# Kernel optimization log

Hardware: AMD Instinct MI355X
Metric: run time of the kernel (lower is better)

The kernel has to match this reference:

```python
import jax, jax.numpy as jnp
import numpy as np

EPS = 1e-7  # eps used inside bbox_iou
LAMBDA_BBOX = 1.0
LAMBDA_CLS = 1.0


def _coords(b):
    x, y, w, h = b[..., 0], b[..., 1], b[..., 2], b[..., 3]
    return x - w / 2, y - h / 2, x + w / 2, y + h / 2


def _pairwise_giou_loss(pred, target):
    # pred [B,T,4] -> [B,T,1,4]; target [B,O,4] -> [B,1,O,4]; broadcast to [B,T,O]
    b1x1, b1y1, b1x2, b1y2 = _coords(pred[:, :, None, :])
    b2x1, b2y1, b2x2, b2y2 = _coords(target[:, None, :, :])
    w1, h1 = b1x2 - b1x1, b1y2 - b1y1 + EPS
    w2, h2 = b2x2 - b2x1, b2y2 - b2y1 + EPS
    inter = jnp.clip(jnp.minimum(b1x2, b2x2) - jnp.maximum(b1x1, b2x1), 0) * \
            jnp.clip(jnp.minimum(b1y2, b2y2) - jnp.maximum(b1y1, b2y1), 0)
    union = w1 * h1 + w2 * h2 - inter + EPS
    iou = inter / union
    cw = jnp.maximum(b1x2, b2x2) - jnp.minimum(b1x1, b2x1)
    ch = jnp.maximum(b1y2, b2y2) - jnp.minimum(b1y1, b2y1)
    c_area = cw * ch + EPS
    giou = iou - (c_area - union) / c_area
    return 1.0 - giou  # [B,T,O]


def _lsa_rows(c):
    # Jonker-Volgenant shortest augmenting path (same algorithm as scipy's
    # linear_sum_assignment). c is [n, m] with n <= m; returns col4row [n].
    n, m = c.shape
    u = np.zeros(n)
    v = np.zeros(m)
    col4row = np.full(n, -1, np.int64)
    row4col = np.full(m, -1, np.int64)
    for cur in range(n):
        shortest = np.full(m, np.inf)
        path = np.full(m, -1, np.int64)
        SR = np.zeros(n, bool)
        SC = np.zeros(m, bool)
        min_val = 0.0
        i = cur
        sink = -1
        while sink == -1:
            SR[i] = True
            r = min_val + c[i] - u[i] - v
            upd = (~SC) & (r < shortest)
            shortest[upd] = r[upd]
            path[upd] = i
            masked = np.where(SC, np.inf, shortest)
            j = int(np.argmin(masked))
            min_val = masked[j]
            SC[j] = True
            if row4col[j] == -1:
                sink = j
            else:
                i = row4col[j]
        u[cur] += min_val
        sr = SR.copy(); sr[cur] = False
        u[sr] += min_val - shortest[col4row[sr]]
        v[SC] -= min_val - shortest[SC]
        j = sink
        while True:
            i = path[j]
            row4col[j] = i
            col4row[i], j = j, col4row[i]
            if i == cur:
                break
    return col4row


def _hungarian_np(cost):
    # Host callback; sequential per-batch like the original scipy loop.
    cost = np.asarray(cost, np.float64)
    B, T, O = cost.shape
    pred_idx = np.zeros((B, O), np.int32)
    tgt_idx = np.zeros((B, O), np.int32)
    for b in range(B):
        col4row = _lsa_rows(cost[b].T)  # assign each target (O rows) a token
        order = np.argsort(col4row)      # sort by pred index like scipy output
        pred_idx[b] = col4row[order].astype(np.int32)
        tgt_idx[b] = order.astype(np.int32)
    return pred_idx, tgt_idx


def _cost_matrix(pred_bboxes, target_bboxes, pred_classes, target_classes):
    B, T, C = pred_classes.shape
    O = target_classes.shape[1]
    log_probs = jax.nn.log_softmax(pred_classes, axis=-1)              # [B,T,C]
    idx = jnp.broadcast_to(target_classes[:, None, :], (B, T, O))      # [B,T,O]
    cls_neg_log = -jnp.take_along_axis(log_probs, idx, axis=-1)        # [B,T,O]
    ciou_loss = _pairwise_giou_loss(pred_bboxes, target_bboxes)        # [B,T,O]
    return LAMBDA_BBOX * ciou_loss + LAMBDA_CLS * cls_neg_log


def setup_inputs() -> dict:
    key = jax.random.key(0)
    k1, k2, k3, k4 = jax.random.split(key, 4)
    B, T, O, C = 32, 2048, 128, 80
    return {
        "pred_bboxes": jax.random.uniform(k1, (B, T, 4), dtype=jnp.float32),
        "target_bboxes": jax.random.uniform(k2, (B, O, 4), dtype=jnp.float32),
        "pred_classes": jax.random.normal(k3, (B, T, C), dtype=jnp.float32),
        "target_classes": jax.random.randint(k4, (B, O), 0, C, dtype=jnp.int32),
    }


def reference(pred_bboxes, target_bboxes, pred_classes, target_classes):
    cost = _cost_matrix(pred_bboxes, target_bboxes, pred_classes, target_classes)
    B, _, O = cost.shape
    out_spec = (jax.ShapeDtypeStruct((B, O), jnp.int32),
                jax.ShapeDtypeStruct((B, O), jnp.int32))
    pred_idx, tgt_idx = jax.pure_callback(_hungarian_np, out_spec, cost)
    return pred_idx, tgt_idx
```

## Files before the change

### kernel.cpp

```cpp
#include <hip/hip_runtime.h>
#include <math.h>
#include <float.h>

#define BB 32
#define TT 2048
#define OO 128
#define CC 80
#define EPSF 1e-7f
#define NT 256
#define SLOTS 8
#define CPAD 81
#define TPT 128
#define NTILE 16

typedef float vf4 __attribute__((ext_vector_type(4)));

struct alignas(16) URow { double u; int row; int pad; };
struct alignas(8)  P2   { int i; int j; };
struct alignas(16) Cand { double v; double u; int j; int row; };

template<int CTRL>
__device__ __forceinline__ void dpp_lexmin(double& bv, int& bj) {
    int lo = __double2loint(bv), hi = __double2hiint(bv);
    int tlo = __builtin_amdgcn_update_dpp(0, lo, CTRL, 0xF, 0xF, false);
    int thi = __builtin_amdgcn_update_dpp(0x7FF00000, hi, CTRL, 0xF, 0xF, false);
    int tj  = __builtin_amdgcn_update_dpp(0x7FFFFFFF, bj, CTRL, 0xF, 0xF, false);
    double tv = __hiloint2double(thi, tlo);
    if (tv <= bv) { bv = tv; bj = tj; }
}

template<int CTRL>
__device__ __forceinline__ void dpp_lexmin_f32(float& bv, int& bj) {
    int tlo = __builtin_amdgcn_update_dpp(0x7F800000, __float_as_int(bv), CTRL, 0xF, 0xF, false);
    int tj  = __builtin_amdgcn_update_dpp(0x7FFFFFFF, bj, CTRL, 0xF, 0xF, false);
    float tv = __int_as_float(tlo);
    if (tv < bv || (tv == bv && tj < bj)) { bv = tv; bj = tj; }
}

union SM {
    struct {
        float  xv[TPT * CPAD];
        float4 box[OO];
        float2 wt[OO];
        unsigned long long rmin[OO * 2];
    } c;
    struct {
        URow   urow[TT];
        P2     path2[TT];
        int    row4col[TT];
        int    claim[TT];
        int    col4row[OO];
        double u[OO];
        int    amin[OO];
        int    flag[OO];
        int    freelist[OO];
        int    selj[OO + 8];
        double selm[OO + 8];
        int    selrow[OO + 8];
        Cand   cand[2][4];
        int    nfree;
    } l;
};

__global__ __launch_bounds__(NT) void hung_fused_kernel(
    const float* __restrict__ pb, const float* __restrict__ tb,
    const float* __restrict__ cls, const int* __restrict__ tcls,
    float* __restrict__ cost, unsigned long long* __restrict__ rowmins,
    int* __restrict__ cnt, int* __restrict__ out) {
#pragma clang fp contract(off)
    __shared__ SM sm;

    int bx = blockIdx.x;
    int b = bx & 31;
    int tile = bx >> 5;
    int t0 = tile * TPT;
    int tid = threadIdx.x;
    int lane = tid & 63;
    int wave = tid >> 6;
    int tok = tid & (TPT - 1);
    int oh = tid >> 7;

    {
        const float* cbase = cls + ((size_t)b * TT + t0) * CC;
        #pragma unroll
        for (int k = 0; k < (TPT * CC) / (NT * 4); ++k) {
            int idx4 = (k * NT + tid) * 4;
            vf4 vv = __builtin_nontemporal_load((const vf4*)(cbase + idx4));
            int r = idx4 / CC;
            int c = idx4 - r * CC;
            float* dst = &sm.c.xv[r * CPAD + c];
            dst[0] = vv.x; dst[1] = vv.y; dst[2] = vv.z; dst[3] = vv.w;
        }
        if (tid < OO) {
            float4 tbox = ((const float4*)tb)[b * OO + tid];
            float x1 = tbox.x - tbox.z / 2.f;
            float y1 = tbox.y - tbox.w / 2.f;
            float x2 = tbox.x + tbox.z / 2.f;
            float y2 = tbox.y + tbox.w / 2.f;
            float4 bb; bb.x = x1; bb.y = y1; bb.z = x2; bb.w = y2;
            sm.c.box[tid] = bb;
            float w2 = x2 - x1;
            float h2 = (y2 - y1) + EPSF;
            float2 wt; wt.x = w2 * h2;
            wt.y = __int_as_float(tcls[b * OO + tid]);
            sm.c.wt[tid] = wt;
        }
        __syncthreads();

        size_t bt = (size_t)b * TT + t0 + tok;
        float4 pbox = ((const float4*)pb)[bt];
        float b1x1 = pbox.x - pbox.z / 2.f;
        float b1y1 = pbox.y - pbox.w / 2.f;
        float b1x2 = pbox.x + pbox.z / 2.f;
        float b1y2 = pbox.y + pbox.w / 2.f;
        float w1 = b1x2 - b1x1;
        float h1 = (b1y2 - b1y1) + EPSF;
        float w1h1 = w1 * h1;

        const float* xr = &sm.c.xv[tok * CPAD];
        float m = xr[0];
        #pragma unroll
        for (int c = 1; c < CC; ++c) m = fmaxf(m, xr[c]);
        float ssum = 0.f;
        #pragma unroll
        for (int c = 0; c < CC; ++c) ssum += expf(xr[c] - m);
        float ls = logf(ssum);

        float* cbt = cost + (size_t)b * OO * TT + t0;
        for (int k = 0; k < OO / 2; ++k) {
            int o = oh * (OO / 2) + k;
            float4 bb = sm.c.box[o];
            float2 wt = sm.c.wt[o];
            float b2x1 = bb.x, b2y1 = bb.y, b2x2 = bb.z, b2y2 = bb.w;
            float iw = fminf(b1x2, b2x2) - fmaxf(b1x1, b2x1);
            float ih = fminf(b1y2, b2y2) - fmaxf(b1y1, b2y1);
            iw = fmaxf(iw, 0.f);
            ih = fmaxf(ih, 0.f);
            float inter = iw * ih;
            float uni = ((w1h1 + wt.x) - inter) + EPSF;
            float iou = inter / uni;
            float cw = fmaxf(b1x2, b2x2) - fminf(b1x1, b2x1);
            float ch = fmaxf(b1y2, b2y2) - fminf(b1y1, b2y1);
            float c_area = (cw * ch) + EPSF;
            float giou = iou - (c_area - uni) / c_area;
            float bbox_loss = 1.0f - giou;

            float xc = xr[__float_as_int(wt.y)];
            float shifted = xc - m;
            float cls_neg = -(shifted - ls);

            float cval = bbox_loss + cls_neg;
            cbt[(size_t)o * TT + tok] = cval;

            float bvv = cval;
            int bjj = t0 + tok;
            dpp_lexmin_f32<0x111>(bvv, bjj);
            dpp_lexmin_f32<0x112>(bvv, bjj);
            dpp_lexmin_f32<0x114>(bvv, bjj);
            dpp_lexmin_f32<0x118>(bvv, bjj);
            dpp_lexmin_f32<0x142>(bvv, bjj);
            dpp_lexmin_f32<0x143>(bvv, bjj);
            if (lane == 63)
                sm.c.rmin[o * 2 + (wave & 1)] =
                    ((unsigned long long)__float_as_uint(bvv) << 32) | (unsigned)bjj;
        }
        __syncthreads();
        if (tid < OO) {
            unsigned long long r0 = sm.c.rmin[tid * 2 + 0];
            unsigned long long r1 = sm.c.rmin[tid * 2 + 1];
            rowmins[((size_t)b * NTILE + tile) * OO + tid] = r0 < r1 ? r0 : r1;
        }
        __syncthreads();
        if (tid == 0)
            __hip_atomic_fetch_add(&cnt[b], 1, __ATOMIC_RELEASE,
                                   __HIP_MEMORY_SCOPE_AGENT);
    }

    if (tile != 0) return;

    if (tid == 0) {
        while (__hip_atomic_load(&cnt[b], __ATOMIC_ACQUIRE,
                                 __HIP_MEMORY_SCOPE_AGENT) < NTILE)
            __builtin_amdgcn_s_sleep(2);
    }
    __syncthreads();

    const float* cb = cost + (size_t)b * OO * TT;
    const int jbase = tid * SLOTS;

    double v_[SLOTS];
    double key[SLOTS];
    #pragma unroll
    for (int s = 0; s < SLOTS; ++s) v_[s] = 0.0;

    if (tid < OO) {
        const unsigned long long* p = rowmins + (size_t)b * NTILE * OO + tid;
        unsigned long long best = p[0];
        #pragma unroll
        for (int t = 1; t < NTILE; ++t) {
            unsigned long long x = p[t * OO];
            if (x < best) best = x;
        }
        sm.l.u[tid] = (double)__uint_as_float((unsigned)(best >> 32));
        sm.l.amin[tid] = (int)(best & 0xFFFFFFFFull);
        sm.l.col4row[tid] = -1;
    }
    for (int j = tid; j < TT; j += NT) { sm.l.row4col[j] = -1; sm.l.claim[j] = 0x7FFFFFFF; }
    __syncthreads();

    if (tid < OO) atomicMin(&sm.l.claim[sm.l.amin[tid]], tid);
    __syncthreads();
    if (tid < OO) {
        int j = sm.l.amin[tid];
        if (sm.l.claim[j] == tid) { sm.l.col4row[tid] = j; sm.l.row4col[j] = tid; }
    }
    __syncthreads();

    for (int j = tid; j < TT; j += NT) {
        int r = sm.l.row4col[j];
        URow t; t.row = r; t.u = (r >= 0) ? sm.l.u[r] : 0.0; t.pad = 0;
        sm.l.urow[j] = t;
    }
    if (tid < OO) sm.l.flag[tid] = (sm.l.col4row[tid] < 0) ? 1 : 0;
    __syncthreads();
    if (tid < OO && sm.l.flag[tid]) {
        int rank = 0;
        for (int o = 0; o < tid; ++o) rank += sm.l.flag[o];
        sm.l.freelist[rank] = tid;
    }
    if (tid == 0) {
        int nf = 0;
        for (int o = 0; o < OO; ++o) nf += sm.l.flag[o];
        sm.l.nfree = nf;
    }
    __syncthreads();
    int nfree = sm.l.nfree;

    float4 pf0, pf1;
    if (nfree > 0) {
        const float* rr = cb + (size_t)sm.l.freelist[0] * TT + jbase;
        pf0 = *(const float4*)rr;
        pf1 = *(const float4*)(rr + 4);
    }

    int par = 0;
    for (int fi = 0; fi < nfree; ++fi) {
        int cur = sm.l.freelist[fi];

        #pragma unroll
        for (int s = 0; s < SLOTS; ++s) key[s] = INFINITY;
        int selbits = 0;
        double mv = 0.0;
        int i = cur, jc = -1;
        double ui = sm.l.u[cur];
        float4 c0 = pf0, c1 = pf1;
        int L = 0, sink;

        while (true) {
            float cv[SLOTS] = {c0.x, c0.y, c0.z, c0.w, c1.x, c1.y, c1.z, c1.w};
            double D = ui - mv;

            double bv = INFINITY;
            int bj = TT;
            #pragma unroll
            for (int s = 0; s < SLOTS; ++s) {
                if (!((selbits >> s) & 1)) {
                    double r = ((double)cv[s] - D) - v_[s];
                    if (r < key[s]) {
                        key[s] = r;
                        P2 p; p.i = i; p.j = jc;
                        sm.l.path2[s * NT + tid] = p;
                    }
                    double kk = key[s];
                    if (kk < bv) { bv = kk; bj = jbase + s; }
                }
            }
            dpp_lexmin<0x111>(bv, bj);
            dpp_lexmin<0x112>(bv, bj);
            dpp_lexmin<0x114>(bv, bj);
            dpp_lexmin<0x118>(bv, bj);
            dpp_lexmin<0x142>(bv, bj);
            dpp_lexmin<0x143>(bv, bj);
            int rlo = __builtin_amdgcn_readlane(__double2loint(bv), 63);
            int rhi = __builtin_amdgcn_readlane(__double2hiint(bv), 63);
            double wv = __hiloint2double(rhi, rlo);
            int wj = __builtin_amdgcn_readlane(bj, 63);

            URow uwv = sm.l.urow[wj];

            par ^= 1;
            if (lane == 0) {
                Cand c; c.v = wv; c.u = uwv.u; c.j = wj; c.row = uwv.row;
                sm.l.cand[par][wave] = c;
            }
            __syncthreads();

            Cand cc0 = sm.l.cand[par][0];
            Cand cc1 = sm.l.cand[par][1];
            Cand cc2 = sm.l.cand[par][2];
            Cand cc3 = sm.l.cand[par][3];
            double MV = cc0.v; int BJ = cc0.j; int WR = cc0.row; double WU = cc0.u;
            if (cc1.v < MV || (cc1.v == MV && cc1.j < BJ)) { MV = cc1.v; BJ = cc1.j; WR = cc1.row; WU = cc1.u; }
            if (cc2.v < MV || (cc2.v == MV && cc2.j < BJ)) { MV = cc2.v; BJ = cc2.j; WR = cc2.row; WU = cc2.u; }
            if (cc3.v < MV || (cc3.v == MV && cc3.j < BJ)) { MV = cc3.v; BJ = cc3.j; WR = cc3.row; WU = cc3.u; }
            mv = MV;
            if ((BJ >> 3) == tid) selbits |= 1 << (BJ & 7);
            if (tid == 0) sm.l.selj[L] = BJ;

            if (WR < 0) { sink = BJ; break; }
            if (tid == 0) { sm.l.selm[L] = MV; sm.l.selrow[L] = WR; }
            i = WR; ui = WU; jc = BJ;
            L++;
            const float* crow = cb + (size_t)i * TT + jbase;
            c0 = *(const float4*)crow;
            c1 = *(const float4*)(crow + 4);
        }

        if (fi + 1 < nfree) {
            const float* rr = cb + (size_t)sm.l.freelist[fi + 1] * TT + jbase;
            pf0 = *(const float4*)rr;
            pf1 = *(const float4*)(rr + 4);
        }

        double M = mv;
        #pragma unroll
        for (int s = 0; s < SLOTS; ++s)
            if ((selbits >> s) & 1) v_[s] = v_[s] - (M - key[s]);
        for (int k = tid; k < L; k += NT)
            sm.l.u[sm.l.selrow[k]] = sm.l.u[sm.l.selrow[k]] + (M - sm.l.selm[k]);
        if (tid == 0) {
            sm.l.u[cur] = sm.l.u[cur] + M;
            int j = sink;
            while (true) {
                P2 p = sm.l.path2[(j & 7) * NT + (j >> 3)];
                int ii = p.i;
                sm.l.row4col[j] = ii;
                sm.l.col4row[ii] = j;
                if (ii == cur) break;
                j = p.j;
            }
        }
        __syncthreads();
        if (tid <= L) {
            int j = sm.l.selj[tid];
            int r = sm.l.row4col[j];
            URow t; t.u = sm.l.u[r]; t.row = r; t.pad = 0;
            sm.l.urow[j] = t;
        }
        __syncthreads();
    }

    if (tid < OO) {
        int my = sm.l.col4row[tid];
        int rank = 0;
        for (int o = 0; o < OO; ++o) rank += (sm.l.col4row[o] < my) ? 1 : 0;
        out[(size_t)b * OO + rank] = my;
        out[(size_t)(BB + b) * OO + rank] = tid;
    }
}

extern "C" void kernel_launch(void* const* d_in, const int* in_sizes, int n_in,
                              void* d_out, int out_size, void* d_ws, size_t ws_size,
                              hipStream_t stream) {
    const float* pred_bboxes = (const float*)d_in[0];
    const float* target_bboxes = (const float*)d_in[1];
    const float* pred_classes = (const float*)d_in[2];
    const int* target_classes = (const int*)d_in[3];
    int* out = (int*)d_out;

    float* cost = (float*)d_ws;
    unsigned long long* rowmins =
        (unsigned long long*)(cost + (size_t)BB * OO * TT);
    int* cnt = (int*)(rowmins + (size_t)BB * NTILE * OO);

    (void)hipMemsetAsync(cnt, 0, BB * sizeof(int), stream);

    hung_fused_kernel<<<BB * NTILE, NT, 0, stream>>>(
        pred_bboxes, target_bboxes, pred_classes, target_classes,
        cost, rowmins, cnt, out);
}
```

Measured before the change: 260.0 us.

## Seed Hungarian init with second-min gaps and dual price adjustments

Each cost row now carries its second-smallest value alongside its minimum through the DPP reductions and the per-tile merge. When several rows share the same argmin column, the row with the largest gap to its second minimum takes that column. The winner's u and the column's v are adjusted by the largest competing gap, so the initial duals stay feasible. The aim is to start with more rows already assigned and tighter duals, which shortens the serial augmenting-path phase. In exchange the reductions do extra shuffle work and the claim step is an O(O^2) scan.

```diff
diff --git a/kernel.cpp b/kernel.cpp
--- a/kernel.cpp
+++ b/kernel.cpp
@@ -30,11 +30,14 @@
 }
 
 template<int CTRL>
-__device__ __forceinline__ void dpp_lexmin_f32(float& bv, int& bj) {
+__device__ __forceinline__ void dpp_top2_f32(float& bv, int& bj, float& sv) {
     int tlo = __builtin_amdgcn_update_dpp(0x7F800000, __float_as_int(bv), CTRL, 0xF, 0xF, false);
     int tj  = __builtin_amdgcn_update_dpp(0x7FFFFFFF, bj, CTRL, 0xF, 0xF, false);
+    int tso = __builtin_amdgcn_update_dpp(0x7F800000, __float_as_int(sv), CTRL, 0xF, 0xF, false);
     float tv = __int_as_float(tlo);
-    if (tv < bv || (tv == bv && tj < bj)) { bv = tv; bj = tj; }
+    float ts = __int_as_float(tso);
+    if (tv < bv || (tv == bv && tj < bj)) { sv = fminf(bv, ts); bv = tv; bj = tj; }
+    else sv = fminf(sv, tv);
 }
 
 union SM {
@@ -43,15 +46,18 @@
         float4 box[OO];
         float2 wt[OO];
         unsigned long long rmin[OO * 2];
+        float  rsec[OO * 2];
     } c;
     struct {
         URow   urow[TT];
         P2     path2[TT];
         int    row4col[TT];
-        int    claim[TT];
         int    col4row[OO];
         double u[OO];
+        double gapd[OO];
+        double pvv[OO];
         int    amin[OO];
+        int    pj[OO];
         int    flag[OO];
         int    freelist[OO];
         int    selj[OO + 8];
@@ -66,7 +72,7 @@
     const float* __restrict__ pb, const float* __restrict__ tb,
     const float* __restrict__ cls, const int* __restrict__ tcls,
     float* __restrict__ cost, unsigned long long* __restrict__ rowmins,
-    int* __restrict__ cnt, int* __restrict__ out) {
+    float* __restrict__ rowsec, int* __restrict__ cnt, int* __restrict__ out) {
 #pragma clang fp contract(off)
     __shared__ SM sm;
 
@@ -154,21 +160,31 @@
 
             float bvv = cval;
             int bjj = t0 + tok;
-            dpp_lexmin_f32<0x111>(bvv, bjj);
-            dpp_lexmin_f32<0x112>(bvv, bjj);
-            dpp_lexmin_f32<0x114>(bvv, bjj);
-            dpp_lexmin_f32<0x118>(bvv, bjj);
-            dpp_lexmin_f32<0x142>(bvv, bjj);
-            dpp_lexmin_f32<0x143>(bvv, bjj);
-            if (lane == 63)
+            float svv = INFINITY;
+            dpp_top2_f32<0x111>(bvv, bjj, svv);
+            dpp_top2_f32<0x112>(bvv, bjj, svv);
+            dpp_top2_f32<0x114>(bvv, bjj, svv);
+            dpp_top2_f32<0x118>(bvv, bjj, svv);
+            dpp_top2_f32<0x142>(bvv, bjj, svv);
+            dpp_top2_f32<0x143>(bvv, bjj, svv);
+            if (lane == 63) {
                 sm.c.rmin[o * 2 + (wave & 1)] =
                     ((unsigned long long)__float_as_uint(bvv) << 32) | (unsigned)bjj;
+                sm.c.rsec[o * 2 + (wave & 1)] = svv;
+            }
         }
         __syncthreads();
         if (tid < OO) {
             unsigned long long r0 = sm.c.rmin[tid * 2 + 0];
             unsigned long long r1 = sm.c.rmin[tid * 2 + 1];
-            rowmins[((size_t)b * NTILE + tile) * OO + tid] = r0 < r1 ? r0 : r1;
+            float s0 = sm.c.rsec[tid * 2 + 0];
+            float s1 = sm.c.rsec[tid * 2 + 1];
+            unsigned long long best; float sec;
+            if (r1 < r0) { best = r1; sec = fminf(s1, __uint_as_float((unsigned)(r0 >> 32))); }
+            else         { best = r0; sec = fminf(s0, __uint_as_float((unsigned)(r1 >> 32))); }
+            size_t off = ((size_t)b * NTILE + tile) * OO + tid;
+            rowmins[off] = best;
+            rowsec[off] = sec;
         }
         __syncthreads();
         if (tid == 0)
@@ -195,26 +211,58 @@
 
     if (tid < OO) {
         const unsigned long long* p = rowmins + (size_t)b * NTILE * OO + tid;
+        const float* ps = rowsec + (size_t)b * NTILE * OO + tid;
         unsigned long long best = p[0];
+        float sec = ps[0];
         #pragma unroll
         for (int t = 1; t < NTILE; ++t) {
-            unsigned long long x = p[t * OO];
-            if (x < best) best = x;
-        }
-        sm.l.u[tid] = (double)__uint_as_float((unsigned)(best >> 32));
+            unsigned long long x = p[(size_t)t * OO];
+            float xs = ps[(size_t)t * OO];
+            if (x < best) { sec = fminf(__uint_as_float((unsigned)(best >> 32)), xs); best = x; }
+            else          { sec = fminf(sec, __uint_as_float((unsigned)(x >> 32))); }
+        }
+        float m1 = __uint_as_float((unsigned)(best >> 32));
+        sm.l.u[tid] = (double)m1;
         sm.l.amin[tid] = (int)(best & 0xFFFFFFFFull);
+        sm.l.gapd[tid] = (double)sec - (double)m1;
         sm.l.col4row[tid] = -1;
     }
-    for (int j = tid; j < TT; j += NT) { sm.l.row4col[j] = -1; sm.l.claim[j] = 0x7FFFFFFF; }
+    for (int j = tid; j < TT; j += NT) sm.l.row4col[j] = -1;
     __syncthreads();
 
-    if (tid < OO) atomicMin(&sm.l.claim[sm.l.amin[tid]], tid);
+    if (tid < OO) {
+        int j1 = sm.l.amin[tid];
+        double g = sm.l.gapd[tid];
+        bool win = true;
+        double p = 0.0;
+        for (int o = 0; o < OO; ++o) {
+            if (o == tid) continue;
+            if (sm.l.amin[o] != j1) continue;
+            double go = sm.l.gapd[o];
+            if (go > g || (go == g && o < tid)) win = false;
+            else p = fmax(p, go);
+        }
+        if (win) {
+            sm.l.col4row[tid] = j1;
+            sm.l.row4col[j1] = tid;
+            sm.l.u[tid] = sm.l.u[tid] + p;
+            sm.l.pj[tid] = j1;
+            sm.l.pvv[tid] = p;
+        } else {
+            sm.l.pj[tid] = -1;
+        }
+    }
     __syncthreads();
-    if (tid < OO) {
-        int j = sm.l.amin[tid];
-        if (sm.l.claim[j] == tid) { sm.l.col4row[tid] = j; sm.l.row4col[j] = tid; }
-    }
-    __syncthreads();
+
+    for (int o = 0; o < OO; ++o) {
+        int pjo = sm.l.pj[o];
+        if ((pjo >> 3) == tid) {
+            double pv = -sm.l.pvv[o];
+            int s = pjo & 7;
+            #pragma unroll
+            for (int ss = 0; ss < SLOTS; ++ss) if (s == ss) v_[ss] = pv;
+        }
+    }
 
     for (int j = tid; j < TT; j += NT) {
         int r = sm.l.row4col[j];
@@ -371,11 +419,12 @@
     float* cost = (float*)d_ws;
     unsigned long long* rowmins =
         (unsigned long long*)(cost + (size_t)BB * OO * TT);
-    int* cnt = (int*)(rowmins + (size_t)BB * NTILE * OO);
+    float* rowsec = (float*)(rowmins + (size_t)BB * NTILE * OO);
+    int* cnt = (int*)(rowsec + (size_t)BB * NTILE * OO);
 
     (void)hipMemsetAsync(cnt, 0, BB * sizeof(int), stream);
 
     hung_fused_kernel<<<BB * NTILE, NT, 0, stream>>>(
         pred_bboxes, target_bboxes, pred_classes, target_classes,
-        cost, rowmins, cnt, out);
+        cost, rowmins, rowsec, cnt, out);
 }
```

After: 283.7 us. 9.1% more time.

## Split fused cost+assignment kernel into two launches, dropping spin-wait counters

Applied to the files above, without the earlier changes.

Splits the single fused kernel, in which tile-0 blocks spin on an atomic counter until all cost tiles finish, into a cost kernel and a separate 32-block assignment kernel launched after it. This removes the memset, the atomics and the spin-wait, and lets each kernel size its shared memory separately. Separate LDS may improve occupancy of the cost phase, since its smaller struct no longer has to match the larger union. The cost is an extra kernel launch and losing the overlap where early-finishing batches could begin assignment before other batches' cost tiles completed.

```diff
diff --git a/kernel.cpp b/kernel.cpp
--- a/kernel.cpp
+++ b/kernel.cpp
@@ -37,38 +37,19 @@
     if (tv < bv || (tv == bv && tj < bj)) { bv = tv; bj = tj; }
 }
 
-union SM {
-    struct {
-        float  xv[TPT * CPAD];
-        float4 box[OO];
-        float2 wt[OO];
-        unsigned long long rmin[OO * 2];
-    } c;
-    struct {
-        URow   urow[TT];
-        P2     path2[TT];
-        int    row4col[TT];
-        int    claim[TT];
-        int    col4row[OO];
-        double u[OO];
-        int    amin[OO];
-        int    flag[OO];
-        int    freelist[OO];
-        int    selj[OO + 8];
-        double selm[OO + 8];
-        int    selrow[OO + 8];
-        Cand   cand[2][4];
-        int    nfree;
-    } l;
+struct SMC {
+    float  xv[TPT * CPAD];
+    float4 box[OO];
+    float2 wt[OO];
+    unsigned long long rmin[OO * 2];
 };
 
-__global__ __launch_bounds__(NT) void hung_fused_kernel(
+__global__ __launch_bounds__(NT) void hung_cost_kernel(
     const float* __restrict__ pb, const float* __restrict__ tb,
     const float* __restrict__ cls, const int* __restrict__ tcls,
-    float* __restrict__ cost, unsigned long long* __restrict__ rowmins,
-    int* __restrict__ cnt, int* __restrict__ out) {
+    float* __restrict__ cost, unsigned long long* __restrict__ rowmins) {
 #pragma clang fp contract(off)
-    __shared__ SM sm;
+    __shared__ SMC sm;
 
     int bx = blockIdx.x;
     int b = bx & 31;
@@ -80,110 +61,125 @@
     int tok = tid & (TPT - 1);
     int oh = tid >> 7;
 
-    {
-        const float* cbase = cls + ((size_t)b * TT + t0) * CC;
-        #pragma unroll
-        for (int k = 0; k < (TPT * CC) / (NT * 4); ++k) {
-            int idx4 = (k * NT + tid) * 4;
-            vf4 vv = __builtin_nontemporal_load((const vf4*)(cbase + idx4));
-            int r = idx4 / CC;
-            int c = idx4 - r * CC;
-            float* dst = &sm.c.xv[r * CPAD + c];
-            dst[0] = vv.x; dst[1] = vv.y; dst[2] = vv.z; dst[3] = vv.w;
-        }
-        if (tid < OO) {
-            float4 tbox = ((const float4*)tb)[b * OO + tid];
-            float x1 = tbox.x - tbox.z / 2.f;
-            float y1 = tbox.y - tbox.w / 2.f;
-            float x2 = tbox.x + tbox.z / 2.f;
-            float y2 = tbox.y + tbox.w / 2.f;
-            float4 bb; bb.x = x1; bb.y = y1; bb.z = x2; bb.w = y2;
-            sm.c.box[tid] = bb;
-            float w2 = x2 - x1;
-            float h2 = (y2 - y1) + EPSF;
-            float2 wt; wt.x = w2 * h2;
-            wt.y = __int_as_float(tcls[b * OO + tid]);
-            sm.c.wt[tid] = wt;
-        }
-        __syncthreads();
-
-        size_t bt = (size_t)b * TT + t0 + tok;
-        float4 pbox = ((const float4*)pb)[bt];
-        float b1x1 = pbox.x - pbox.z / 2.f;
-        float b1y1 = pbox.y - pbox.w / 2.f;
-        float b1x2 = pbox.x + pbox.z / 2.f;
-        float b1y2 = pbox.y + pbox.w / 2.f;
-        float w1 = b1x2 - b1x1;
-        float h1 = (b1y2 - b1y1) + EPSF;
-        float w1h1 = w1 * h1;
-
-        const float* xr = &sm.c.xv[tok * CPAD];
-        float m = xr[0];
-        #pragma unroll
-        for (int c = 1; c < CC; ++c) m = fmaxf(m, xr[c]);
-        float ssum = 0.f;
-        #pragma unroll
-        for (int c = 0; c < CC; ++c) ssum += expf(xr[c] - m);
-        float ls = logf(ssum);
-
-        float* cbt = cost + (size_t)b * OO * TT + t0;
-        for (int k = 0; k < OO / 2; ++k) {
-            int o = oh * (OO / 2) + k;
-            float4 bb = sm.c.box[o];
-            float2 wt = sm.c.wt[o];
-            float b2x1 = bb.x, b2y1 = bb.y, b2x2 = bb.z, b2y2 = bb.w;
-            float iw = fminf(b1x2, b2x2) - fmaxf(b1x1, b2x1);
-            float ih = fminf(b1y2, b2y2) - fmaxf(b1y1, b2y1);
-            iw = fmaxf(iw, 0.f);
-            ih = fmaxf(ih, 0.f);
-            float inter = iw * ih;
-            float uni = ((w1h1 + wt.x) - inter) + EPSF;
-            float iou = inter / uni;
-            float cw = fmaxf(b1x2, b2x2) - fminf(b1x1, b2x1);
-            float ch = fmaxf(b1y2, b2y2) - fminf(b1y1, b2y1);
-            float c_area = (cw * ch) + EPSF;
-            float giou = iou - (c_area - uni) / c_area;
-            float bbox_loss = 1.0f - giou;
-
-            float xc = xr[__float_as_int(wt.y)];
-            float shifted = xc - m;
-            float cls_neg = -(shifted - ls);
-
-            float cval = bbox_loss + cls_neg;
-            cbt[(size_t)o * TT + tok] = cval;
-
-            float bvv = cval;
-            int bjj = t0 + tok;
-            dpp_lexmin_f32<0x111>(bvv, bjj);
-            dpp_lexmin_f32<0x112>(bvv, bjj);
-            dpp_lexmin_f32<0x114>(bvv, bjj);
-            dpp_lexmin_f32<0x118>(bvv, bjj);
-            dpp_lexmin_f32<0x142>(bvv, bjj);
-            dpp_lexmin_f32<0x143>(bvv, bjj);
-            if (lane == 63)
-                sm.c.rmin[o * 2 + (wave & 1)] =
-                    ((unsigned long long)__float_as_uint(bvv) << 32) | (unsigned)bjj;
-        }
-        __syncthreads();
-        if (tid < OO) {
-            unsigned long long r0 = sm.c.rmin[tid * 2 + 0];
-            unsigned long long r1 = sm.c.rmin[tid * 2 + 1];
-            rowmins[((size_t)b * NTILE + tile) * OO + tid] = r0 < r1 ? r0 : r1;
-        }
-        __syncthreads();
-        if (tid == 0)
-            __hip_atomic_fetch_add(&cnt[b], 1, __ATOMIC_RELEASE,
-                                   __HIP_MEMORY_SCOPE_AGENT);
-    }
-
-    if (tile != 0) return;
-
-    if (tid == 0) {
-        while (__hip_atomic_load(&cnt[b], __ATOMIC_ACQUIRE,
-                                 __HIP_MEMORY_SCOPE_AGENT) < NTILE)
-            __builtin_amdgcn_s_sleep(2);
-    }
-    __syncthreads();
+    const float* cbase = cls + ((size_t)b * TT + t0) * CC;
+    #pragma unroll
+    for (int k = 0; k < (TPT * CC) / (NT * 4); ++k) {
+        int idx4 = (k * NT + tid) * 4;
+        vf4 vv = __builtin_nontemporal_load((const vf4*)(cbase + idx4));
+        int r = idx4 / CC;
+        int c = idx4 - r * CC;
+        float* dst = &sm.xv[r * CPAD + c];
+        dst[0] = vv.x; dst[1] = vv.y; dst[2] = vv.z; dst[3] = vv.w;
+    }
+    if (tid < OO) {
+        float4 tbox = ((const float4*)tb)[b * OO + tid];
+        float x1 = tbox.x - tbox.z / 2.f;
+        float y1 = tbox.y - tbox.w / 2.f;
+        float x2 = tbox.x + tbox.z / 2.f;
+        float y2 = tbox.y + tbox.w / 2.f;
+        float4 bb; bb.x = x1; bb.y = y1; bb.z = x2; bb.w = y2;
+        sm.box[tid] = bb;
+        float w2 = x2 - x1;
+        float h2 = (y2 - y1) + EPSF;
+        float2 wt; wt.x = w2 * h2;
+        wt.y = __int_as_float(tcls[b * OO + tid]);
+        sm.wt[tid] = wt;
+    }
+    __syncthreads();
+
+    size_t bt = (size_t)b * TT + t0 + tok;
+    float4 pbox = ((const float4*)pb)[bt];
+    float b1x1 = pbox.x - pbox.z / 2.f;
+    float b1y1 = pbox.y - pbox.w / 2.f;
+    float b1x2 = pbox.x + pbox.z / 2.f;
+    float b1y2 = pbox.y + pbox.w / 2.f;
+    float w1 = b1x2 - b1x1;
+    float h1 = (b1y2 - b1y1) + EPSF;
+    float w1h1 = w1 * h1;
+
+    const float* xr = &sm.xv[tok * CPAD];
+    float m = xr[0];
+    #pragma unroll
+    for (int c = 1; c < CC; ++c) m = fmaxf(m, xr[c]);
+    float ssum = 0.f;
+    #pragma unroll
+    for (int c = 0; c < CC; ++c) ssum += expf(xr[c] - m);
+    float ls = logf(ssum);
+
+    float* cbt = cost + (size_t)b * OO * TT + t0;
+    for (int k = 0; k < OO / 2; ++k) {
+        int o = oh * (OO / 2) + k;
+        float4 bb = sm.box[o];
+        float2 wt = sm.wt[o];
+        float b2x1 = bb.x, b2y1 = bb.y, b2x2 = bb.z, b2y2 = bb.w;
+        float iw = fminf(b1x2, b2x2) - fmaxf(b1x1, b2x1);
+        float ih = fminf(b1y2, b2y2) - fmaxf(b1y1, b2y1);
+        iw = fmaxf(iw, 0.f);
+        ih = fmaxf(ih, 0.f);
+        float inter = iw * ih;
+        float uni = ((w1h1 + wt.x) - inter) + EPSF;
+        float iou = inter / uni;
+        float cw = fmaxf(b1x2, b2x2) - fminf(b1x1, b2x1);
+        float ch = fmaxf(b1y2, b2y2) - fminf(b1y1, b2y1);
+        float c_area = (cw * ch) + EPSF;
+        float giou = iou - (c_area - uni) / c_area;
+        float bbox_loss = 1.0f - giou;
+
+        float xc = xr[__float_as_int(wt.y)];
+        float shifted = xc - m;
+        float cls_neg = -(shifted - ls);
+
+        float cval = bbox_loss + cls_neg;
+        cbt[(size_t)o * TT + tok] = cval;
+
+        float bvv = cval;
+        int bjj = t0 + tok;
+        dpp_lexmin_f32<0x111>(bvv, bjj);
+        dpp_lexmin_f32<0x112>(bvv, bjj);
+        dpp_lexmin_f32<0x114>(bvv, bjj);
+        dpp_lexmin_f32<0x118>(bvv, bjj);
+        dpp_lexmin_f32<0x142>(bvv, bjj);
+        dpp_lexmin_f32<0x143>(bvv, bjj);
+        if (lane == 63)
+            sm.rmin[o * 2 + (wave & 1)] =
+                ((unsigned long long)__float_as_uint(bvv) << 32) | (unsigned)bjj;
+    }
+    __syncthreads();
+    if (tid < OO) {
+        unsigned long long r0 = sm.rmin[tid * 2 + 0];
+        unsigned long long r1 = sm.rmin[tid * 2 + 1];
+        rowmins[((size_t)b * NTILE + tile) * OO + tid] = r0 < r1 ? r0 : r1;
+    }
+}
+
+struct SML {
+    URow   urow[TT];
+    P2     path2[TT];
+    int    row4col[TT];
+    int    claim[TT];
+    int    col4row[OO];
+    double u[OO];
+    int    amin[OO];
+    int    flag[OO];
+    int    freelist[OO];
+    int    selj[OO + 8];
+    double selm[OO + 8];
+    int    selrow[OO + 8];
+    Cand   cand[2][4];
+    int    nfree;
+};
+
+__global__ __launch_bounds__(NT) void hung_lsa_kernel(
+    const float* __restrict__ cost,
+    const unsigned long long* __restrict__ rowmins,
+    int* __restrict__ out) {
+#pragma clang fp contract(off)
+    __shared__ SML sm;
+
+    int b = blockIdx.x;
+    int tid = threadIdx.x;
+    int lane = tid & 63;
+    int wave = tid >> 6;
 
     const float* cb = cost + (size_t)b * OO * TT;
     const int jbase = tid * SLOTS;
@@ -198,61 +194,61 @@
         unsigned long long best = p[0];
         #pragma unroll
         for (int t = 1; t < NTILE; ++t) {
-            unsigned long long x = p[t * OO];
+            unsigned long long x = p[(size_t)t * OO];
             if (x < best) best = x;
         }
-        sm.l.u[tid] = (double)__uint_as_float((unsigned)(best >> 32));
-        sm.l.amin[tid] = (int)(best & 0xFFFFFFFFull);
-        sm.l.col4row[tid] = -1;
-    }
-    for (int j = tid; j < TT; j += NT) { sm.l.row4col[j] = -1; sm.l.claim[j] = 0x7FFFFFFF; }
-    __syncthreads();
-
-    if (tid < OO) atomicMin(&sm.l.claim[sm.l.amin[tid]], tid);
-    __syncthreads();
-    if (tid < OO) {
-        int j = sm.l.amin[tid];
-        if (sm.l.claim[j] == tid) { sm.l.col4row[tid] = j; sm.l.row4col[j] = tid; }
+        sm.u[tid] = (double)__uint_as_float((unsigned)(best >> 32));
+        sm.amin[tid] = (int)(best & 0xFFFFFFFFull);
+        sm.col4row[tid] = -1;
+    }
+    for (int j = tid; j < TT; j += NT) { sm.row4col[j] = -1; sm.claim[j] = 0x7FFFFFFF; }
+    __syncthreads();
+
+    if (tid < OO) atomicMin(&sm.claim[sm.amin[tid]], tid);
+    __syncthreads();
+    if (tid < OO) {
+        int j = sm.amin[tid];
+        if (sm.claim[j] == tid) { sm.col4row[tid] = j; sm.row4col[j] = tid; }
     }
     __syncthreads();
 
     for (int j = tid; j < TT; j += NT) {
-        int r = sm.l.row4col[j];
-        URow t; t.row = r; t.u = (r >= 0) ? sm.l.u[r] : 0.0; t.pad = 0;
-        sm.l.urow[j] = t;
-    }
-    if (tid < OO) sm.l.flag[tid] = (sm.l.col4row[tid] < 0) ? 1 : 0;
-    __syncthreads();
-    if (tid < OO && sm.l.flag[tid]) {
+        int r = sm.row4col[j];
+        URow t; t.row = r; t.u = (r >= 0) ? sm.u[r] : 0.0; t.pad = 0;
+        sm.urow[j] = t;
+    }
+    if (tid < OO) sm.flag[tid] = (sm.col4row[tid] < 0) ? 1 : 0;
+    __syncthreads();
+    if (tid < OO && sm.flag[tid]) {
         int rank = 0;
-        for (int o = 0; o < tid; ++o) rank += sm.l.flag[o];
-        sm.l.freelist[rank] = tid;
+        for (int o = 0; o < tid; ++o) rank += sm.flag[o];
+        sm.freelist[rank] = tid;
     }
     if (tid == 0) {
         int nf = 0;
-        for (int o = 0; o < OO; ++o) nf += sm.l.flag[o];
-        sm.l.nfree = nf;
-    }
-    __syncthreads();
-    int nfree = sm.l.nfree;
+        for (int o = 0; o < OO; ++o) nf += sm.flag[o];
+        sm.nfree = nf;
+    }
+    __syncthreads();
+    int nfree = sm.nfree;
 
     float4 pf0, pf1;
     if (nfree > 0) {
-        const float* rr = cb + (size_t)sm.l.freelist[0] * TT + jbase;
+        const float* rr = cb + (size_t)sm.freelist[0] * TT + jbase;
         pf0 = *(const float4*)rr;
         pf1 = *(const float4*)(rr + 4);
     }
 
     int par = 0;
     for (int fi = 0; fi < nfree; ++fi) {
-        int cur = sm.l.freelist[fi];
+        int cur = sm.freelist[fi];
 
         #pragma unroll
         for (int s = 0; s < SLOTS; ++s) key[s] = INFINITY;
         int selbits = 0;
         double mv = 0.0;
         int i = cur, jc = -1;
-        double ui = sm.l.u[cur];
+        double ui = sm.u[cur];
         float4 c0 = pf0, c1 = pf1;
         int L = 0, sink;
 
@@ -269,7 +265,7 @@
                     if (r < key[s]) {
                         key[s] = r;
                         P2 p; p.i = i; p.j = jc;
-                        sm.l.path2[s * NT + tid] = p;
+                        sm.path2[s * NT + tid] = p;
                     }
                     double kk = key[s];
                     if (kk < bv) { bv = kk; bj = jbase + s; }
@@ -286,29 +282,29 @@
             double wv = __hiloint2double(rhi, rlo);
             int wj = __builtin_amdgcn_readlane(bj, 63);
 
-            URow uwv = sm.l.urow[wj];
+            URow uwv = sm.urow[wj];
 
             par ^= 1;
             if (lane == 0) {
                 Cand c; c.v = wv; c.u = uwv.u; c.j = wj; c.row = uwv.row;
-                sm.l.cand[par][wave] = c;
+                sm.cand[par][wave] = c;
             }
             __syncthreads();
 
-            Cand cc0 = sm.l.cand[par][0];
-            Cand cc1 = sm.l.cand[par][1];
-            Cand cc2 = sm.l.cand[par][2];
-            Cand cc3 = sm.l.cand[par][3];
+            Cand cc0 = sm.cand[par][0];
+            Cand cc1 = sm.cand[par][1];
+            Cand cc2 = sm.cand[par][2];
+            Cand cc3 = sm.cand[par][3];
             double MV = cc0.v; int BJ = cc0.j; int WR = cc0.row; double WU = cc0.u;
             if (cc1.v < MV || (cc1.v == MV && cc1.j < BJ)) { MV = cc1.v; BJ = cc1.j; WR = cc1.row; WU = cc1.u; }
             if (cc2.v < MV || (cc2.v == MV && cc2.j < BJ)) { MV = cc2.v; BJ = cc2.j; WR = cc2.row; WU = cc2.u; }
             if (cc3.v < MV || (cc3.v == MV && cc3.j < BJ)) { MV = cc3.v; BJ = cc3.j; WR = cc3.row; WU = cc3.u; }
             mv = MV;
             if ((BJ >> 3) == tid) selbits |= 1 << (BJ & 7);
-            if (tid == 0) sm.l.selj[L] = BJ;
+            if (tid == 0) sm.selj[L] = BJ;
 
             if (WR < 0) { sink = BJ; break; }
-            if (tid == 0) { sm.l.selm[L] = MV; sm.l.selrow[L] = WR; }
+            if (tid == 0) { sm.selm[L] = MV; sm.selrow[L] = WR; }
             i = WR; ui = WU; jc = BJ;
             L++;
             const float* crow = cb + (size_t)i * TT + jbase;
@@ -317,7 +313,7 @@
         }
 
         if (fi + 1 < nfree) {
-            const float* rr = cb + (size_t)sm.l.freelist[fi + 1] * TT + jbase;
+            const float* rr = cb + (size_t)sm.freelist[fi + 1] * TT + jbase;
             pf0 = *(const float4*)rr;
             pf1 = *(const float4*)(rr + 4);
         }
@@ -327,33 +323,33 @@
         for (int s = 0; s < SLOTS; ++s)
             if ((selbits >> s) & 1) v_[s] = v_[s] - (M - key[s]);
         for (int k = tid; k < L; k += NT)
-            sm.l.u[sm.l.selrow[k]] = sm.l.u[sm.l.selrow[k]] + (M - sm.l.selm[k]);
+            sm.u[sm.selrow[k]] = sm.u[sm.selrow[k]] + (M - sm.selm[k]);
         if (tid == 0) {
-            sm.l.u[cur] = sm.l.u[cur] + M;
+            sm.u[cur] = sm.u[cur] + M;
             int j = sink;
             while (true) {
-                P2 p = sm.l.path2[(j & 7) * NT + (j >> 3)];
+                P2 p = sm.path2[(j & 7) * NT + (j >> 3)];
                 int ii = p.i;
-                sm.l.row4col[j] = ii;
-                sm.l.col4row[ii] = j;
+                sm.row4col[j] = ii;
+                sm.col4row[ii] = j;
                 if (ii == cur) break;
                 j = p.j;
             }
         }
         __syncthreads();
         if (tid <= L) {
-            int j = sm.l.selj[tid];
-            int r = sm.l.row4col[j];
-            URow t; t.u = sm.l.u[r]; t.row = r; t.pad = 0;
-            sm.l.urow[j] = t;
+            int j = sm.selj[tid];
+            int r = sm.row4col[j];
+            URow t; t.u = sm.u[r]; t.row = r; t.pad = 0;
+            sm.urow[j] = t;
         }
         __syncthreads();
     }
 
     if (tid < OO) {
-        int my = sm.l.col4row[tid];
+        int my = sm.col4row[tid];
         int rank = 0;
-        for (int o = 0; o < OO; ++o) rank += (sm.l.col4row[o] < my) ? 1 : 0;
+        for (int o = 0; o < OO; ++o) rank += (sm.col4row[o] < my) ? 1 : 0;
         out[(size_t)b * OO + rank] = my;
         out[(size_t)(BB + b) * OO + rank] = tid;
     }
@@ -371,11 +367,8 @@
     float* cost = (float*)d_ws;
     unsigned long long* rowmins =
         (unsigned long long*)(cost + (size_t)BB * OO * TT);
-    int* cnt = (int*)(rowmins + (size_t)BB * NTILE * OO);
-
-    (void)hipMemsetAsync(cnt, 0, BB * sizeof(int), stream);
-
-    hung_fused_kernel<<<BB * NTILE, NT, 0, stream>>>(
-        pred_bboxes, target_bboxes, pred_classes, target_classes,
-        cost, rowmins, cnt, out);
-}
+
+    hung_cost_kernel<<<BB * NTILE, NT, 0, stream>>>(
+        pred_bboxes, target_bboxes, pred_classes, target_classes, cost, rowmins);
+    hung_lsa_kernel<<<BB, NT, 0, stream>>>(cost, rowmins, out);
+}
```

Measured after the change: 253.6 us. -2.5%, faster.
